# Performance work log

Hardware: AMD Instinct MI355X
Metric: run time of the kernel (lower is better)

## Reference

```python
import jax, jax.numpy as jnp
import numpy as np

HID = 1024
DEPTH = 2

def _rhn_layer(x, Win, bin_, Wh, bh, Wt, bt):
    # x: [B, T, in]; returns outputs [B, T, H]
    B = x.shape[0]
    h0 = jnp.zeros((B, HID), dtype=x.dtype)
    xt = jnp.swapaxes(x, 0, 1)  # [T, B, in]

    def step(h_prev, x_t):
        h = x_t @ Win + bin_
        for i in range(DEPTH):
            t_gate = jax.nn.sigmoid(h @ Wt[i] + bt[i])
            h_layer = jnp.tanh(h @ Wh[i] + bh[i])
            h = t_gate * h_layer + (1.0 - t_gate) * h
        h_new = h + h_prev
        return h_new, h_new

    _, outs = jax.lax.scan(step, h0, xt)  # [T, B, H]
    return jnp.swapaxes(outs, 0, 1)


def setup_inputs() -> dict:
    key = jax.random.key(0)
    ks = jax.random.split(key, 16)
    B, T, IN, H, OUT = 64, 256, 128, HID, 128
    s = lambda fan_in: 1.0 / np.sqrt(fan_in)
    d = {}
    d["x"] = jax.random.normal(ks[0], (B, T, IN), dtype=jnp.float32)
    # layer 0 (input_size=IN)
    d["l0_Win"] = jax.random.uniform(ks[1], (IN, H), minval=-s(IN), maxval=s(IN))
    d["l0_bin"] = jax.random.uniform(ks[2], (H,), minval=-s(IN), maxval=s(IN))
    d["l0_Wh"] = jax.random.uniform(ks[3], (DEPTH, H, H), minval=-s(H), maxval=s(H))
    d["l0_bh"] = jax.random.uniform(ks[4], (DEPTH, H), minval=-s(H), maxval=s(H))
    d["l0_Wt"] = jax.random.uniform(ks[5], (DEPTH, H, H), minval=-s(H), maxval=s(H))
    d["l0_bt"] = jax.random.uniform(ks[6], (DEPTH, H), minval=-s(H), maxval=s(H))
    # layer 1 (input_size=H)
    d["l1_Win"] = jax.random.uniform(ks[7], (H, H), minval=-s(H), maxval=s(H))
    d["l1_bin"] = jax.random.uniform(ks[8], (H,), minval=-s(H), maxval=s(H))
    d["l1_Wh"] = jax.random.uniform(ks[9], (DEPTH, H, H), minval=-s(H), maxval=s(H))
    d["l1_bh"] = jax.random.uniform(ks[10], (DEPTH, H), minval=-s(H), maxval=s(H))
    d["l1_Wt"] = jax.random.uniform(ks[11], (DEPTH, H, H), minval=-s(H), maxval=s(H))
    d["l1_bt"] = jax.random.uniform(ks[12], (DEPTH, H), minval=-s(H), maxval=s(H))
    # final fc
    d["fc_W"] = jax.random.uniform(ks[13], (H, OUT), minval=-s(H), maxval=s(H))
    d["fc_b"] = jax.random.uniform(ks[14], (OUT,), minval=-s(H), maxval=s(H))
    return d


def reference(x, l0_Win, l0_bin, l0_Wh, l0_bh, l0_Wt, l0_bt,
              l1_Win, l1_bin, l1_Wh, l1_bh, l1_Wt, l1_bt, fc_W, fc_b):
    out = _rhn_layer(x, l0_Win, l0_bin, l0_Wh, l0_bh, l0_Wt, l0_bt)
    out = _rhn_layer(out, l1_Win, l1_bin, l1_Wh, l1_bh, l1_Wt, l1_bt)
    # forecast_horizon = 1 -> last time step only
    out = out[:, -1:, :] @ fc_W + fc_b  # [B, 1, OUT]
    return out
```

## Files before the change

### kernel.cpp

```cpp
#include <hip/hip_runtime.h>

typedef unsigned short u16;
typedef unsigned int u32;
typedef __bf16 bf16x8 __attribute__((ext_vector_type(8)));
typedef float floatx4 __attribute__((ext_vector_type(4)));

#define HID 1024
#define BATCH 64
#define SEQ 256
#define INDIM 128
#define OUTDIM 128
#define MROWS (BATCH*SEQ)

__device__ __forceinline__ float b2f(u16 u) {
    union { u32 u; float f; } v; v.u = ((u32)u) << 16; return v.f;
}
__device__ __forceinline__ u16 f2b(float f) {
    union { float f; u32 u; } v; v.f = f;
    u32 x = v.u;
    x += 0x7fffu + ((x >> 16) & 1u);
    return (u16)(x >> 16);
}
__device__ __forceinline__ float sigm(float x) { return 1.f / (1.f + __expf(-x)); }
__device__ __forceinline__ float tanh_f(float x) { return 2.f / (1.f + __expf(-2.f * x)) - 1.f; }

__device__ __forceinline__ void gld16(const u16* g, u16* l) {
    __builtin_amdgcn_global_load_lds(
        (const __attribute__((address_space(1))) void*)g,
        (__attribute__((address_space(3))) void*)l, 16, 0, 0);
}

__global__ void detect_dtype(const u16* __restrict__ w, int* __restrict__ flag) {
    __shared__ int s;
    if (threadIdx.x == 0) s = 0;
    __syncthreads();
    int bad = 0;
    for (int i = threadIdx.x; i < 4096; i += 256) {
        int e = (w[i] >> 7) & 0xff;
        if (e >= 127) bad = 1;
    }
    if (bad) atomicOr(&s, 1);
    __syncthreads();
    if (threadIdx.x == 0) *flag = s;
}

struct CvtList { const void* s[7]; u16* d[7]; int n[7]; };

__global__ void convert7(CvtList C, const int* __restrict__ flag) {
    const int fp32 = *flag;
    const int z = blockIdx.y;
    const int n = C.n[z];
    const int stride = gridDim.x * 256;
    for (int i = blockIdx.x * 256 + threadIdx.x; i < n; i += stride) {
        u16 o;
        if (fp32) o = f2b(((const float*)C.s[z])[i]);
        else      o = ((const u16*)C.s[z])[i];
        C.d[z][i] = o;
    }
}

struct TListO {
    const void* s[10];
    u16*        d[10];
    int         R[10];
    int         Cc[10];
    long        off[10];
};

__global__ void transpose10(TListO L, const int* __restrict__ flag) {
    const int fp32 = *flag;
    const int z = blockIdx.z;
    const void* src = L.s[z];
    u16*        dst = L.d[z];
    const int R  = L.R[z];
    const int Cc = L.Cc[z];
    const long zo = L.off[z];
    const int tr = blockIdx.y * 32, tc = blockIdx.x * 32;
    if (tr >= R || tc >= Cc) return;
    __align__(16) __shared__ u16 t[32][33];
    const int tx = threadIdx.x, ty = threadIdx.y;
#pragma unroll
    for (int i = 0; i < 4; ++i) {
        const int r = ty + i * 8;
        const long e = zo + (long)(tr + r) * Cc + tc + tx;
        u16 v;
        if (fp32) v = f2b(((const float*)src)[e]);
        else      v = ((const u16*)src)[e];
        t[r][tx] = v;
    }
    __syncthreads();
#pragma unroll
    for (int i = 0; i < 4; ++i) {
        const int r = ty + i * 8;
        dst[(size_t)(tc + r) * R + tr + tx] = t[tx][r];
    }
}

__device__ __forceinline__ void tile_swizzle(int& m0, int& n0) {
    const int lin = blockIdx.y * gridDim.x + blockIdx.x;
    const int xcd = lin & 7;
    const int loc = lin >> 3;
    m0 = (xcd * 16 + (loc & 15)) * 128;
    n0 = (loc >> 4) * 128;
}

__global__ __launch_bounds__(256, 2) void gemm128(
    const u16* __restrict__ A, const u16* __restrict__ BT,
    const u16* __restrict__ bias, u16* __restrict__ C,
    int M, int N, int K)
{
    __align__(16) __shared__ u16 As[128 * 64];
    __align__(16) __shared__ u16 Bs[128 * 64];

    const int tid  = threadIdx.x;
    const int lane = tid & 63;
    const int wid  = tid >> 6;
    const int wr   = wid >> 1;
    const int wc   = wid & 1;

    int m0, n0;
    tile_swizzle(m0, n0);

    floatx4 acc[4][4] = {};

    const int srow = lane >> 3;
    const int scol = 8 * ((lane & 7) ^ (lane >> 3));
    const int cb   = wid * 4;
    const u16* Ag[4]; const u16* Bg[4];
    u16 *Al[4], *Bl[4];
#pragma unroll
    for (int j = 0; j < 4; ++j) {
        const int c = cb + j;
        const int r = c * 8 + srow;
        Ag[j] = A  + (size_t)(m0 + r) * K + scol;
        Bg[j] = BT + (size_t)(n0 + r) * K + scol;
        Al[j] = As + c * 512;
        Bl[j] = Bs + c * 512;
    }

    const int quad = lane >> 4;
    const int l16  = lane & 15;
    const int swz  = l16 & 7;

    const int nk = K >> 6;
    for (int kt = 0; kt < nk; ++kt) {
        __syncthreads();
#pragma unroll
        for (int j = 0; j < 4; ++j) {
            gld16(Ag[j], Al[j]);  gld16(Bg[j], Bl[j]);
            Ag[j] += 64; Bg[j] += 64;
        }
        __syncthreads();

#pragma unroll
        for (int kk = 0; kk < 2; ++kk) {
            const int slot = ((kk * 4 + quad) ^ swz) * 8;
            bf16x8 af[4], bfr[4];
#pragma unroll
            for (int i = 0; i < 4; ++i) {
                af[i]  = *(const bf16x8*)(As + (wr * 64 + i * 16 + l16) * 64 + slot);
                bfr[i] = *(const bf16x8*)(Bs + (wc * 64 + i * 16 + l16) * 64 + slot);
            }
#pragma unroll
            for (int i = 0; i < 4; ++i)
#pragma unroll
                for (int j = 0; j < 4; ++j)
                    acc[i][j] = __builtin_amdgcn_mfma_f32_16x16x32_bf16(af[i], bfr[j], acc[i][j], 0, 0, 0);
        }
    }

#pragma unroll
    for (int i = 0; i < 4; ++i) {
        const int rowb = m0 + wr * 64 + i * 16 + quad * 4;
#pragma unroll
        for (int j = 0; j < 4; ++j) {
            const int col = n0 + wc * 64 + j * 16 + l16;
            const float bv = b2f(bias[col]);
#pragma unroll
            for (int r = 0; r < 4; ++r)
                C[(size_t)(rowb + r) * N + col] = f2b(acc[i][j][r] + bv);
        }
    }
}

__global__ __launch_bounds__(256, 3) void gemm_hw(
    const u16* __restrict__ A,
    const u16* __restrict__ WtT,
    const u16* __restrict__ WhT,
    const u16* __restrict__ bt, const u16* __restrict__ bh,
    u16* __restrict__ Hout,
    int M, int N, int K)
{
    __align__(16) __shared__ u16 As [128 * 64];
    __align__(16) __shared__ u16 Bts[64 * 64];
    __align__(16) __shared__ u16 Bhs[64 * 64];

    const int tid  = threadIdx.x;
    const int lane = tid & 63;
    const int wid  = tid >> 6;

    const int lin = blockIdx.y * gridDim.x + blockIdx.x;
    const int xcd = lin & 7;
    const int loc = lin >> 3;
    const int m0 = (xcd * 16 + (loc & 15)) * 128;
    const int n0 = (loc >> 4) * 64;

    floatx4 acct[2][4] = {};
    floatx4 acch[2][4] = {};

    const int srow = lane >> 3;
    const int scol = 8 * ((lane & 7) ^ (lane >> 3));
    const u16* Ag[4]; const u16* Tg[2]; const u16* Hg[2];
    u16 *Al[4], *Tl[2], *Hl[2];
#pragma unroll
    for (int j = 0; j < 4; ++j) {
        const int c = wid * 4 + j;
        Ag[j] = A + (size_t)(m0 + c * 8 + srow) * K + scol;
        Al[j] = As + c * 512;
    }
#pragma unroll
    for (int j = 0; j < 2; ++j) {
        const int c = wid * 2 + j;
        Tg[j] = WtT + (size_t)(n0 + c * 8 + srow) * K + scol;
        Hg[j] = WhT + (size_t)(n0 + c * 8 + srow) * K + scol;
        Tl[j] = Bts + c * 512;
        Hl[j] = Bhs + c * 512;
    }

    const int quad = lane >> 4;
    const int l16  = lane & 15;
    const int swz  = l16 & 7;

    const int nk = K >> 6;
    for (int kt = 0; kt < nk; ++kt) {
        __syncthreads();
#pragma unroll
        for (int j = 0; j < 4; ++j) { gld16(Ag[j], Al[j]); Ag[j] += 64; }
#pragma unroll
        for (int j = 0; j < 2; ++j) {
            gld16(Tg[j], Tl[j]); Tg[j] += 64;
            gld16(Hg[j], Hl[j]); Hg[j] += 64;
        }
        __syncthreads();

#pragma unroll
        for (int kk = 0; kk < 2; ++kk) {
            const int slot = ((kk * 4 + quad) ^ swz) * 8;
            bf16x8 af[2], btf[4], bhf[4];
#pragma unroll
            for (int i = 0; i < 2; ++i)
                af[i] = *(const bf16x8*)(As + (wid * 32 + i * 16 + l16) * 64 + slot);
#pragma unroll
            for (int j = 0; j < 4; ++j) {
                btf[j] = *(const bf16x8*)(Bts + (j * 16 + l16) * 64 + slot);
                bhf[j] = *(const bf16x8*)(Bhs + (j * 16 + l16) * 64 + slot);
            }
#pragma unroll
            for (int i = 0; i < 2; ++i)
#pragma unroll
                for (int j = 0; j < 4; ++j) {
                    acct[i][j] = __builtin_amdgcn_mfma_f32_16x16x32_bf16(af[i], btf[j], acct[i][j], 0, 0, 0);
                    acch[i][j] = __builtin_amdgcn_mfma_f32_16x16x32_bf16(af[i], bhf[j], acch[i][j], 0, 0, 0);
                }
        }
    }

#pragma unroll
    for (int i = 0; i < 2; ++i) {
        const int rowb = m0 + wid * 32 + i * 16 + quad * 4;
#pragma unroll
        for (int j = 0; j < 4; ++j) {
            const int col = n0 + j * 16 + l16;
            const float btv = b2f(bt[col]);
            const float bhv = b2f(bh[col]);
#pragma unroll
            for (int r = 0; r < 4; ++r) {
                const size_t idx = (size_t)(rowb + r) * N + col;
                const float hold = b2f(A[idx]);
                const float tg = sigm(acct[i][j][r] + btv);
                const float hl = tanh_f(acch[i][j][r] + bhv);
                Hout[idx] = f2b(hold + tg * (hl - hold));
            }
        }
    }
}

__global__ void cumsum_t(u16* g) {
    const int id = blockIdx.x * 256 + threadIdx.x;
    const int b = id >> 10, f = id & 1023;
    size_t base = (size_t)b * SEQ * HID + f;
    float acc = 0.f;
#pragma unroll 4
    for (int t = 0; t < SEQ; ++t) {
        size_t idx = base + (size_t)t * HID;
        acc += b2f(g[idx]);
        g[idx] = f2b(acc);
    }
}

__global__ void sum_t(const u16* __restrict__ g, float* __restrict__ out) {
    const int id = blockIdx.x * 256 + threadIdx.x;
    const int b = id >> 10, f = id & 1023;
    size_t base = (size_t)b * SEQ * HID + f;
    float acc = 0.f;
#pragma unroll 4
    for (int t = 0; t < SEQ; ++t)
        acc += b2f(g[base + (size_t)t * HID]);
    out[id] = acc;
}

__global__ void fc_final(const float* __restrict__ hf, const void* __restrict__ W,
                         const void* __restrict__ bias, void* __restrict__ out,
                         const int* __restrict__ flag) {
    __shared__ float sh[HID];
    const int fp32 = *flag;
    const int b = blockIdx.x, o = threadIdx.x;
    for (int k = o; k < HID; k += 128) sh[k] = hf[(size_t)b * HID + k];
    __syncthreads();
    float acc;
    if (fp32) {
        acc = ((const float*)bias)[o];
        for (int k = 0; k < HID; ++k)
            acc += sh[k] * ((const float*)W)[(size_t)k * OUTDIM + o];
        ((float*)out)[b * OUTDIM + o] = acc;
    } else {
        acc = b2f(((const u16*)bias)[o]);
        for (int k = 0; k < HID; ++k)
            acc += sh[k] * b2f(((const u16*)W)[(size_t)k * OUTDIM + o]);
        ((u16*)out)[b * OUTDIM + o] = f2b(acc);
    }
}

extern "C" void kernel_launch(void* const* d_in, const int* in_sizes, int n_in,
                              void* d_out, int out_size, void* d_ws, size_t ws_size,
                              hipStream_t stream) {
    const void* x      = d_in[0];
    const void* l0_Win = d_in[1];
    const void* l0_bin = d_in[2];
    const void* l0_Wh  = d_in[3];
    const void* l0_bh  = d_in[4];
    const void* l0_Wt  = d_in[5];
    const void* l0_bt  = d_in[6];
    const void* l1_Win = d_in[7];
    const void* l1_bin = d_in[8];
    const void* l1_Wh  = d_in[9];
    const void* l1_bh  = d_in[10];
    const void* l1_Wt  = d_in[11];
    const void* l1_bt  = d_in[12];
    const void* fc_W   = d_in[13];
    const void* fc_b   = d_in[14];

    char* ws = (char*)d_ws;
    u16* Pa = (u16*)(ws);
    u16* Pb = (u16*)(ws + 33554432);
    u16* xc = Pb;
    u16* tW = (u16*)(ws + 67108864);
    u16* tWin0 = tW;
    u16* tWt00 = tWin0 + 131072;
    u16* tWt01 = tWt00 + 1048576;
    u16* tWh00 = tWt01 + 1048576;
    u16* tWh01 = tWh00 + 1048576;
    u16* tWin1 = tWh01 + 1048576;
    u16* tWt10 = tWin1 + 1048576;
    u16* tWt11 = tWt10 + 1048576;
    u16* tWh10 = tWt11 + 1048576;
    u16* tWh11 = tWh10 + 1048576;
    u16* smallb = tWh11 + 1048576;
    u16* binc0 = smallb;
    u16* bhc0  = binc0 + 1024;
    u16* btc0  = bhc0 + 2048;
    u16* binc1 = btc0 + 2048;
    u16* bhc1  = binc1 + 1024;
    u16* btc1  = bhc1 + 2048;
    int* flag  = (int*)(btc1 + 2048);
    float* hfinal = (float*)Pa;

    detect_dtype<<<1, 256, 0, stream>>>((const u16*)l0_Wh, flag);

    const long DD = (long)HID * HID;
    TListO L;
    L.s[0] = l0_Win; L.d[0] = tWin0; L.R[0] = INDIM; L.Cc[0] = HID; L.off[0] = 0;
    L.s[1] = l0_Wt;  L.d[1] = tWt00; L.R[1] = HID;   L.Cc[1] = HID; L.off[1] = 0;
    L.s[2] = l0_Wt;  L.d[2] = tWt01; L.R[2] = HID;   L.Cc[2] = HID; L.off[2] = DD;
    L.s[3] = l0_Wh;  L.d[3] = tWh00; L.R[3] = HID;   L.Cc[3] = HID; L.off[3] = 0;
    L.s[4] = l0_Wh;  L.d[4] = tWh01; L.R[4] = HID;   L.Cc[4] = HID; L.off[4] = DD;
    L.s[5] = l1_Win; L.d[5] = tWin1; L.R[5] = HID;   L.Cc[5] = HID; L.off[5] = 0;
    L.s[6] = l1_Wt;  L.d[6] = tWt10; L.R[6] = HID;   L.Cc[6] = HID; L.off[6] = 0;
    L.s[7] = l1_Wt;  L.d[7] = tWt11; L.R[7] = HID;   L.Cc[7] = HID; L.off[7] = DD;
    L.s[8] = l1_Wh;  L.d[8] = tWh10; L.R[8] = HID;   L.Cc[8] = HID; L.off[8] = 0;
    L.s[9] = l1_Wh;  L.d[9] = tWh11; L.R[9] = HID;   L.Cc[9] = HID; L.off[9] = DD;
    transpose10<<<dim3(32, 32, 10), dim3(32, 8), 0, stream>>>(L, flag);

    CvtList C7;
    C7.s[0] = x;      C7.d[0] = xc;    C7.n[0] = MROWS * INDIM;
    C7.s[1] = l0_bin; C7.d[1] = binc0; C7.n[1] = HID;
    C7.s[2] = l0_bh;  C7.d[2] = bhc0;  C7.n[2] = 2 * HID;
    C7.s[3] = l0_bt;  C7.d[3] = btc0;  C7.n[3] = 2 * HID;
    C7.s[4] = l1_bin; C7.d[4] = binc1; C7.n[4] = HID;
    C7.s[5] = l1_bh;  C7.d[5] = bhc1;  C7.n[5] = 2 * HID;
    C7.s[6] = l1_bt;  C7.d[6] = btc1;  C7.n[6] = 2 * HID;
    convert7<<<dim3(512, 7), 256, 0, stream>>>(C7, flag);

    gemm128<<<dim3(8, 128), 256, 0, stream>>>(xc, tWin0, binc0, Pa, MROWS, HID, INDIM);
    gemm_hw<<<dim3(16, 128), 256, 0, stream>>>(Pa, tWt00, tWh00, btc0, bhc0, Pb, MROWS, HID, HID);
    gemm_hw<<<dim3(16, 128), 256, 0, stream>>>(Pb, tWt01, tWh01, btc0 + HID, bhc0 + HID, Pa, MROWS, HID, HID);
    cumsum_t<<<256, 256, 0, stream>>>(Pa);

    gemm128<<<dim3(8, 128), 256, 0, stream>>>(Pa, tWin1, binc1, Pb, MROWS, HID, HID);
    gemm_hw<<<dim3(16, 128), 256, 0, stream>>>(Pb, tWt10, tWh10, btc1, bhc1, Pa, MROWS, HID, HID);
    gemm_hw<<<dim3(16, 128), 256, 0, stream>>>(Pa, tWt11, tWh11, btc1 + HID, bhc1 + HID, Pb, MROWS, HID, HID);

    sum_t<<<256, 256, 0, stream>>>(Pb, hfinal);
    fc_final<<<64, 128, 0, stream>>>(hfinal, fc_W, fc_b, d_out, flag);
}
```

Baseline: 523.9 us.

## Merge prep kernels, split time cumsum into two-pass scan, narrower-tile layer-1 input GEMM

Folds dtype detection, weight transposes and bias/input conversion into one launch by detecting the dtype inline with a wave ballot. The sequential cumsum over 256 time steps is split into a chunked two-pass scan, giving four times more threads. The layer-1 input projection now uses a new 128x64-tile GEMM with XCD-aware block mapping, so more blocks can be resident. This costs extra passes over the activation buffer for the scan and re-probes the dtype in every block.

```diff
diff --git a/kernel.cpp b/kernel.cpp
--- a/kernel.cpp
+++ b/kernel.cpp
@@ -30,48 +30,39 @@
         (__attribute__((address_space(3))) void*)l, 16, 0, 0);
 }
 
-__global__ void detect_dtype(const u16* __restrict__ w, int* __restrict__ flag) {
-    __shared__ int s;
-    if (threadIdx.x == 0) s = 0;
-    __syncthreads();
-    int bad = 0;
-    for (int i = threadIdx.x; i < 4096; i += 256) {
-        int e = (w[i] >> 7) & 0xff;
-        if (e >= 127) bad = 1;
-    }
-    if (bad) atomicOr(&s, 1);
-    __syncthreads();
-    if (threadIdx.x == 0) *flag = s;
-}
-
-struct CvtList { const void* s[7]; u16* d[7]; int n[7]; };
-
-__global__ void convert7(CvtList C, const int* __restrict__ flag) {
-    const int fp32 = *flag;
-    const int z = blockIdx.y;
-    const int n = C.n[z];
-    const int stride = gridDim.x * 256;
-    for (int i = blockIdx.x * 256 + threadIdx.x; i < n; i += stride) {
-        u16 o;
-        if (fp32) o = f2b(((const float*)C.s[z])[i]);
-        else      o = ((const u16*)C.s[z])[i];
-        C.d[z][i] = o;
-    }
-}
-
-struct TListO {
-    const void* s[10];
-    u16*        d[10];
-    int         R[10];
-    int         Cc[10];
-    long        off[10];
+__device__ __forceinline__ int is_fp32(const u16* probe) {
+    const int lane = threadIdx.x & 63;
+    const int e = (probe[lane * 7] >> 7) & 0xff;
+    return __ballot(e >= 127) != 0ULL;
+}
+
+struct PrepList {
+    const void* s[17];
+    u16*        d[17];
+    int         R[17];
+    int         Cc[17];
+    long        off[17];
+    const u16*  probe;
 };
 
-__global__ void transpose10(TListO L, const int* __restrict__ flag) {
-    const int fp32 = *flag;
+__global__ void prep_all(PrepList L) {
+    const int fp32 = is_fp32(L.probe);
     const int z = blockIdx.z;
     const void* src = L.s[z];
     u16*        dst = L.d[z];
+    if (z >= 10) {
+        const int n = L.R[z];
+        const int tid = threadIdx.y * 32 + threadIdx.x;
+        const int blk = blockIdx.y * 32 + blockIdx.x;
+        const int stride = 1024 * 256;
+        for (int i = blk * 256 + tid; i < n; i += stride) {
+            u16 o;
+            if (fp32) o = f2b(((const float*)src)[i]);
+            else      o = ((const u16*)src)[i];
+            dst[i] = o;
+        }
+        return;
+    }
     const int R  = L.R[z];
     const int Cc = L.Cc[z];
     const long zo = L.off[z];
@@ -175,6 +166,88 @@
 #pragma unroll
         for (int j = 0; j < 4; ++j) {
             const int col = n0 + wc * 64 + j * 16 + l16;
+            const float bv = b2f(bias[col]);
+#pragma unroll
+            for (int r = 0; r < 4; ++r)
+                C[(size_t)(rowb + r) * N + col] = f2b(acc[i][j][r] + bv);
+        }
+    }
+}
+
+__global__ __launch_bounds__(256, 4) void gemm64n(
+    const u16* __restrict__ A, const u16* __restrict__ BT,
+    const u16* __restrict__ bias, u16* __restrict__ C,
+    int M, int N, int K)
+{
+    __align__(16) __shared__ u16 As[128 * 64];
+    __align__(16) __shared__ u16 Bs[64 * 64];
+
+    const int tid  = threadIdx.x;
+    const int lane = tid & 63;
+    const int wid  = tid >> 6;
+
+    const int lin = blockIdx.y * gridDim.x + blockIdx.x;
+    const int xcd = lin & 7;
+    const int loc = lin >> 3;
+    const int m0 = (xcd * 16 + (loc & 15)) * 128;
+    const int n0 = (loc >> 4) * 64;
+
+    floatx4 acc[2][4] = {};
+
+    const int srow = lane >> 3;
+    const int scol = 8 * ((lane & 7) ^ (lane >> 3));
+    const u16* Ag[4]; const u16* Bg[2];
+    u16 *Al[4], *Bl[2];
+#pragma unroll
+    for (int j = 0; j < 4; ++j) {
+        const int c = wid * 4 + j;
+        Ag[j] = A + (size_t)(m0 + c * 8 + srow) * K + scol;
+        Al[j] = As + c * 512;
+    }
+#pragma unroll
+    for (int j = 0; j < 2; ++j) {
+        const int c = wid * 2 + j;
+        Bg[j] = BT + (size_t)(n0 + c * 8 + srow) * K + scol;
+        Bl[j] = Bs + c * 512;
+    }
+
+    const int quad = lane >> 4;
+    const int l16  = lane & 15;
+    const int swz  = l16 & 7;
+
+    const int nk = K >> 6;
+    for (int kt = 0; kt < nk; ++kt) {
+        __syncthreads();
+#pragma unroll
+        for (int j = 0; j < 4; ++j) { gld16(Ag[j], Al[j]); Ag[j] += 64; }
+#pragma unroll
+        for (int j = 0; j < 2; ++j) { gld16(Bg[j], Bl[j]); Bg[j] += 64; }
+        __syncthreads();
+
+#pragma unroll
+        for (int kk = 0; kk < 2; ++kk) {
+            const int slot = ((kk * 4 + quad) ^ swz) * 8;
+            bf16x8 af[2], bf[4];
+#pragma unroll
+            for (int i = 0; i < 2; ++i)
+                af[i] = *(const bf16x8*)(As + (wid * 32 + i * 16 + l16) * 64 + slot);
+#pragma unroll
+            for (int j = 0; j < 4; ++j)
+                bf[j] = *(const bf16x8*)(Bs + (j * 16 + l16) * 64 + slot);
+#pragma unroll
+            for (int i = 0; i < 2; ++i)
+#pragma unroll
+                for (int j = 0; j < 4; ++j)
+                    acc[i][j] = __builtin_amdgcn_mfma_f32_16x16x32_bf16(af[i], bf[j], acc[i][j], 0, 0, 0);
+        }
+    }
+
+#pragma unroll
+    for (int i = 0; i < 2; ++i) {
+        const int rowb = m0 + wid * 32 + i * 16 + quad * 4;
+#pragma unroll
+        for (int j = 0; j < 4; ++j) {
+            const int col = n0 + j * 16 + l16;
             const float bv = b2f(bias[col]);
 #pragma unroll
             for (int r = 0; r < 4; ++r)
@@ -285,16 +358,29 @@
     }
 }
 
-__global__ void cumsum_t(u16* g) {
+__global__ void scan_pass1(const u16* __restrict__ g, float* __restrict__ partial) {
     const int id = blockIdx.x * 256 + threadIdx.x;
-    const int b = id >> 10, f = id & 1023;
-    size_t base = (size_t)b * SEQ * HID + f;
-    float acc = 0.f;
+    const int f = id & 1023, c = (id >> 10) & 3, b = id >> 12;
+    size_t base = (size_t)b * SEQ * HID + (size_t)c * 64 * HID + f;
+    float s = 0.f;
 #pragma unroll 4
-    for (int t = 0; t < SEQ; ++t) {
+    for (int t = 0; t < 64; ++t)
+        s += b2f(g[base + (size_t)t * HID]);
+    partial[id] = s;
+}
+
+__global__ void scan_pass2(u16* __restrict__ g, const float* __restrict__ partial) {
+    const int id = blockIdx.x * 256 + threadIdx.x;
+    const int f = id & 1023, c = (id >> 10) & 3, b = id >> 12;
+    float run = 0.f;
+    for (int cc = 0; cc < c; ++cc)
+        run += partial[(b << 12) + (cc << 10) + f];
+    size_t base = (size_t)b * SEQ * HID + (size_t)c * 64 * HID + f;
+#pragma unroll 4
+    for (int t = 0; t < 64; ++t) {
         size_t idx = base + (size_t)t * HID;
-        acc += b2f(g[idx]);
-        g[idx] = f2b(acc);
+        run += b2f(g[idx]);
+        g[idx] = f2b(run);
     }
 }
 
@@ -310,10 +396,9 @@
 }
 
 __global__ void fc_final(const float* __restrict__ hf, const void* __restrict__ W,
-                         const void* __restrict__ bias, void* __restrict__ out,
-                         const int* __restrict__ flag) {
+                         const void* __restrict__ bias, void* __restrict__ out) {
     __shared__ float sh[HID];
-    const int fp32 = *flag;
+    const int fp32 = is_fp32((const u16*)W);
     const int b = blockIdx.x, o = threadIdx.x;
     for (int k = o; k < HID; k += 128) sh[k] = hf[(size_t)b * HID + k];
     __syncthreads();
@@ -372,13 +457,10 @@
     u16* binc1 = btc0 + 2048;
     u16* bhc1  = binc1 + 1024;
     u16* btc1  = bhc1 + 2048;
-    int* flag  = (int*)(btc1 + 2048);
     float* hfinal = (float*)Pa;
 
-    detect_dtype<<<1, 256, 0, stream>>>((const u16*)l0_Wh, flag);
-
     const long DD = (long)HID * HID;
-    TListO L;
+    PrepList L;
     L.s[0] = l0_Win; L.d[0] = tWin0; L.R[0] = INDIM; L.Cc[0] = HID; L.off[0] = 0;
     L.s[1] = l0_Wt;  L.d[1] = tWt00; L.R[1] = HID;   L.Cc[1] = HID; L.off[1] = 0;
     L.s[2] = l0_Wt;  L.d[2] = tWt01; L.R[2] = HID;   L.Cc[2] = HID; L.off[2] = DD;
@@ -389,27 +471,27 @@
     L.s[7] = l1_Wt;  L.d[7] = tWt11; L.R[7] = HID;   L.Cc[7] = HID; L.off[7] = DD;
     L.s[8] = l1_Wh;  L.d[8] = tWh10; L.R[8] = HID;   L.Cc[8] = HID; L.off[8] = 0;
     L.s[9] = l1_Wh;  L.d[9] = tWh11; L.R[9] = HID;   L.Cc[9] = HID; L.off[9] = DD;
-    transpose10<<<dim3(32, 32, 10), dim3(32, 8), 0, stream>>>(L, flag);
-
-    CvtList C7;
-    C7.s[0] = x;      C7.d[0] = xc;    C7.n[0] = MROWS * INDIM;
-    C7.s[1] = l0_bin; C7.d[1] = binc0; C7.n[1] = HID;
-    C7.s[2] = l0_bh;  C7.d[2] = bhc0;  C7.n[2] = 2 * HID;
-    C7.s[3] = l0_bt;  C7.d[3] = btc0;  C7.n[3] = 2 * HID;
-    C7.s[4] = l1_bin; C7.d[4] = binc1; C7.n[4] = HID;
-    C7.s[5] = l1_bh;  C7.d[5] = bhc1;  C7.n[5] = 2 * HID;
-    C7.s[6] = l1_bt;  C7.d[6] = btc1;  C7.n[6] = 2 * HID;
-    convert7<<<dim3(512, 7), 256, 0, stream>>>(C7, flag);
+    L.s[10] = x;      L.d[10] = xc;    L.R[10] = MROWS * INDIM; L.Cc[10] = 0; L.off[10] = 0;
+    L.s[11] = l0_bin; L.d[11] = binc0; L.R[11] = HID;     L.Cc[11] = 0; L.off[11] = 0;
+    L.s[12] = l0_bh;  L.d[12] = bhc0;  L.R[12] = 2 * HID; L.Cc[12] = 0; L.off[12] = 0;
+    L.s[13] = l0_bt;  L.d[13] = btc0;  L.R[13] = 2 * HID; L.Cc[13] = 0; L.off[13] = 0;
+    L.s[14] = l1_bin; L.d[14] = binc1; L.R[14] = HID;     L.Cc[14] = 0; L.off[14] = 0;
+    L.s[15] = l1_bh;  L.d[15] = bhc1;  L.R[15] = 2 * HID; L.Cc[15] = 0; L.off[15] = 0;
+    L.s[16] = l1_bt;  L.d[16] = btc1;  L.R[16] = 2 * HID; L.Cc[16] = 0; L.off[16] = 0;
+    L.probe = (const u16*)l0_Wh;
+
+    prep_all<<<dim3(32, 32, 17), dim3(32, 8), 0, stream>>>(L);
 
     gemm128<<<dim3(8, 128), 256, 0, stream>>>(xc, tWin0, binc0, Pa, MROWS, HID, INDIM);
     gemm_hw<<<dim3(16, 128), 256, 0, stream>>>(Pa, tWt00, tWh00, btc0, bhc0, Pb, MROWS, HID, HID);
     gemm_hw<<<dim3(16, 128), 256, 0, stream>>>(Pb, tWt01, tWh01, btc0 + HID, bhc0 + HID, Pa, MROWS, HID, HID);
-    cumsum_t<<<256, 256, 0, stream>>>(Pa);
-
-    gemm128<<<dim3(8, 128), 256, 0, stream>>>(Pa, tWin1, binc1, Pb, MROWS, HID, HID);
+    scan_pass1<<<1024, 256, 0, stream>>>(Pa, (float*)Pb);
+    scan_pass2<<<1024, 256, 0, stream>>>(Pa, (const float*)Pb);
+
+    gemm64n<<<dim3(16, 128), 256, 0, stream>>>(Pa, tWin1, binc1, Pb, MROWS, HID, HID);
     gemm_hw<<<dim3(16, 128), 256, 0, stream>>>(Pb, tWt10, tWh10, btc1, bhc1, Pa, MROWS, HID, HID);
     gemm_hw<<<dim3(16, 128), 256, 0, stream>>>(Pa, tWt11, tWh11, btc1 + HID, bhc1 + HID, Pb, MROWS, HID, HID);
 
     sum_t<<<256, 256, 0, stream>>>(Pb, hfinal);
-    fc_final<<<64, 128, 0, stream>>>(hfinal, fc_W, fc_b, d_out, flag);
-}
+    fc_final<<<64, 128, 0, stream>>>(hfinal, fc_W, fc_b, d_out);
+}
```

Measured after the change: 549.4 us. +4.9%, slower.
